# Kernel tuning notes

Measured on AMD Instinct MI355X. Metric: run time of the kernel, lower is better.

## Reference

```python
import jax, jax.numpy as jnp
import numpy as np

B, N, C, H = 2, 2048, 1024, 16
D = C // H  # head_dim = 64
ROPE_THETA = 500000.0
INIT_STD = 0.02


def setup_inputs() -> dict:
    key = jax.random.key(0)
    ks = jax.random.split(key, 6)
    hidden_states = jax.random.normal(ks[0], (B, N, C), dtype=jnp.float32)
    # rotary embeddings: standard llama-style, built from rope_theta
    inv_freq = jnp.asarray(1.0 / (ROPE_THETA ** (np.arange(0, D, 2, dtype=np.float32) / D)), jnp.float32)
    freqs = jnp.outer(jnp.arange(N, dtype=jnp.float32), inv_freq)  # (N, D/2)
    emb = jnp.concatenate([freqs, freqs], axis=-1)  # (N, D)
    cos = jnp.broadcast_to(jnp.cos(emb)[None], (B, N, D))
    sin = jnp.broadcast_to(jnp.sin(emb)[None], (B, N, D))
    Wq = jax.random.normal(ks[1], (C, C), jnp.float32) * INIT_STD
    Wk = jax.random.normal(ks[2], (C, C), jnp.float32) * INIT_STD
    Wv = jax.random.normal(ks[3], (C, C), jnp.float32) * INIT_STD
    Wo = jax.random.normal(ks[4], (C, C), jnp.float32) * INIT_STD
    return {"hidden_states": hidden_states, "cos": cos, "sin": sin,
            "Wq": Wq, "Wk": Wk, "Wv": Wv, "Wo": Wo}


def _rotate_half(x):
    x1, x2 = x[..., : D // 2], x[..., D // 2 :]
    return jnp.concatenate((-x2, x1), axis=-1)


def reference(hidden_states, cos, sin, Wq, Wk, Wv, Wo):
    scaling = D ** -0.5
    # projections; W stored as (in, out) so y = x @ W
    q = (hidden_states @ Wq) * scaling
    k = hidden_states @ Wk
    v = hidden_states @ Wv
    q = q.reshape(B, N, H, D)
    k = k.reshape(B, N, H, D)
    v = v.reshape(B, N, H, D)
    # RoPE, cos/sin broadcast over heads: (B,N,1,D)
    c = cos[:, :, None, :]
    s = sin[:, :, None, :]
    q = q * c + _rotate_half(q) * s
    k = k * c + _rotate_half(k) * s
    # causal SDPA (q already scaled)
    scores = jnp.einsum("bqhd,bkhd->bhqk", q, k)  # (B,H,N,N)
    causal = jnp.tril(jnp.ones((N, N), dtype=bool))
    scores = jnp.where(causal[None, None], scores, jnp.finfo(scores.dtype).min)
    probs = jax.nn.softmax(scores, axis=-1)
    out = jnp.einsum("bhqk,bkhd->bqhd", probs, v).reshape(B, N, C)
    return out @ Wo
```

## Files before the change

kernel.cpp:

```cpp
#include <hip/hip_runtime.h>
#include <hip/hip_bf16.h>

typedef __hip_bfloat16 bf16;
typedef __attribute__((ext_vector_type(8))) short short8;
typedef __attribute__((ext_vector_type(4))) short short4v;
typedef __attribute__((ext_vector_type(4))) float f32x4;

#define BB 2
#define NN 2048
#define CC 1024
#define HH 16
#define DD 64
#define MM (BB*NN)
#define QKVN 3072
#define LOG2E 1.44269504088896340736f

__device__ __forceinline__ void glds16(const void* g, void* l) {
    __builtin_amdgcn_global_load_lds((const __attribute__((address_space(1))) void*)g,
                                     (__attribute__((address_space(3))) void*)l, 16, 0, 0);
}
__device__ __forceinline__ short pkbf(float x) { bf16 t = (bf16)x; return *(short*)&t; }
__device__ __forceinline__ float b2f(short s) {
    return __uint_as_float(((unsigned)(unsigned short)s) << 16);
}

__global__ __launch_bounds__(256) void prep_fused(const float* __restrict__ hs,
                                                  const float* __restrict__ W0,
                                                  const float* __restrict__ W1,
                                                  const float* __restrict__ W2,
                                                  const float* __restrict__ W3,
                                                  bf16* __restrict__ hsb,
                                                  bf16* __restrict__ Wtqkv,
                                                  bf16* __restrict__ Wto) {
    __shared__ float t[32][33];
    const int bid = blockIdx.x;
    if (bid < 4096) {
        const int i = bid * 256 + threadIdx.x;
        float4 v = ((const float4*)hs)[i];
        short4v s;
        s.x = pkbf(v.x); s.y = pkbf(v.y); s.z = pkbf(v.z); s.w = pkbf(v.w);
        *((short4v*)hsb + i) = s;
    } else {
        const int b2 = bid - 4096;
        const int z = b2 >> 10;
        const float* W = z == 0 ? W0 : (z == 1 ? W1 : (z == 2 ? W2 : W3));
        bf16* dst = z < 3 ? Wtqkv + (size_t)z * CC * CC : Wto;
        const int bx = b2 & 31, by = (b2 >> 5) & 31;
        const int tx = threadIdx.x & 31, ty = threadIdx.x >> 5;
        const int x0 = bx * 32, y0 = by * 32;
        #pragma unroll
        for (int i = 0; i < 4; ++i)
            t[ty + i * 8][tx] = W[(size_t)(y0 + ty + i * 8) * CC + x0 + tx];
        __syncthreads();
        #pragma unroll
        for (int i = 0; i < 4; ++i)
            dst[(size_t)(x0 + ty + i * 8) * CC + y0 + tx] = (bf16)t[tx][ty + i * 8];
    }
}

__global__ __launch_bounds__(256) void gemm4qkv(const bf16* __restrict__ A,
                                                const bf16* __restrict__ Bt,
                                                bf16* __restrict__ Cb,
                                                const float* __restrict__ cosp,
                                                const float* __restrict__ sinp,
                                                bf16* __restrict__ VtOut) {
    __shared__ __align__(16) bf16 As[3][128 * 32];
    __shared__ __align__(16) bf16 Bs[3][128 * 32];
    const int tid = threadIdx.x, lane = tid & 63, wid = tid >> 6;
    const int wr = wid >> 1, wc = wid & 1, l16 = lane & 15, lg = lane >> 4;
    const int n0 = blockIdx.x * 128, m0 = blockIdx.y * 128;

    f32x4 acc[4][4];
    #pragma unroll
    for (int i = 0; i < 4; ++i)
        #pragma unroll
        for (int j = 0; j < 4; ++j) acc[i][j] = {0.f, 0.f, 0.f, 0.f};

    const int issue0 = wid * 2;
    const int sr0 = (issue0 * 1024 + lane * 16) >> 6;
    const int sc0 = ((issue0 * 1024 + lane * 16) & 63) >> 1;
    const int sr1 = ((issue0 + 1) * 1024 + lane * 16) >> 6;
    const int sc1 = (((issue0 + 1) * 1024 + lane * 16) & 63) >> 1;

    auto stage = [&](int k0, int bufi) {
        glds16(&A [(size_t)(m0 + sr0) * 1024 + k0 + sc0], (char*)&As[bufi][0] + issue0 * 1024);
        glds16(&Bt[(size_t)(n0 + sr0) * 1024 + k0 + sc0], (char*)&Bs[bufi][0] + issue0 * 1024);
        glds16(&A [(size_t)(m0 + sr1) * 1024 + k0 + sc1], (char*)&As[bufi][0] + (issue0 + 1) * 1024);
        glds16(&Bt[(size_t)(n0 + sr1) * 1024 + k0 + sc1], (char*)&Bs[bufi][0] + (issue0 + 1) * 1024);
    };

    stage(0, 0);
    stage(32, 1);
    int cur = 0, sb = 2;
    for (int t = 0; t < 32; ++t) {
        asm volatile("s_waitcnt vmcnt(4)" ::: "memory");
        __builtin_amdgcn_s_barrier();
        __builtin_amdgcn_sched_barrier(0);
        if (t + 2 < 32) stage((t + 2) * 32, sb);
        short8 af[4], bfr[4];
        #pragma unroll
        for (int i = 0; i < 4; ++i) af[i]  = *(const short8*)((char*)&As[cur][0] + (wr * 64 + i * 16 + l16) * 64 + lg * 16);
        #pragma unroll
        for (int j = 0; j < 4; ++j) bfr[j] = *(const short8*)((char*)&Bs[cur][0] + (wc * 64 + j * 16 + l16) * 64 + lg * 16);
        #pragma unroll
        for (int i = 0; i < 4; ++i)
            #pragma unroll
            for (int j = 0; j < 4; ++j)
                acc[i][j] = __builtin_amdgcn_mfma_f32_16x16x32_bf16(af[i], bfr[j], acc[i][j], 0, 0, 0);
        cur = (cur == 2) ? 0 : cur + 1;
        sb  = (sb  == 2) ? 0 : sb  + 1;
    }

    if (n0 >= 2 * CC) {
        #pragma unroll
        for (int i = 0; i < 4; ++i) {
            const int row0 = m0 + wr * 64 + i * 16 + lg * 4;
            const int bb = row0 >> 11, nn_ = row0 & (NN - 1);
            #pragma unroll
            for (int j = 0; j < 4; ++j) {
                const int col = n0 - 2 * CC + wc * 64 + j * 16 + l16;
                const int hh = col >> 6, d = col & 63;
                short4v s4;
                #pragma unroll
                for (int r = 0; r < 4; ++r) s4[r] = pkbf(acc[i][j][r]);
                *(short4v*)&VtOut[((size_t)(bb * HH + hh) * DD + d) * NN + nn_] = s4;
            }
        }
    } else {
        const float qs = (n0 < CC) ? 0.125f * LOG2E : 1.0f;
        #pragma unroll
        for (int i = 0; i < 4; ++i)
            #pragma unroll
            for (int r = 0; r < 4; ++r) {
                const int row = m0 + wr * 64 + i * 16 + lg * 4 + r;
                #pragma unroll
                for (int j = 0; j < 2; ++j) {
                    const int d = j * 16 + l16;
                    const float cv = cosp[(size_t)row * DD + d];
                    const float sv = sinp[(size_t)row * DD + d];
                    const float x1 = acc[i][j][r];
                    const float x2 = acc[i][j + 2][r];
                    const size_t cbase = (size_t)row * QKVN + n0 + wc * 64 + j * 16 + l16;
                    Cb[cbase]      = (bf16)((x1 * cv - x2 * sv) * qs);
                    Cb[cbase + 32] = (bf16)((x2 * cv + x1 * sv) * qs);
                }
            }
    }
}

__global__ __launch_bounds__(256) void gemm4o(const bf16* __restrict__ A,
                                              const bf16* __restrict__ Bt,
                                              float* __restrict__ Cf) {
    __shared__ __align__(16) bf16 As[3][64 * 32];
    __shared__ __align__(16) bf16 Bs[3][128 * 32];
    const int tid = threadIdx.x, lane = tid & 63, wid = tid >> 6;
    const int wr = wid >> 1, wc = wid & 1, l16 = lane & 15, lg = lane >> 4;
    const int n0 = blockIdx.x * 128, m0 = blockIdx.y * 64;

    f32x4 acc[2][4];
    #pragma unroll
    for (int i = 0; i < 2; ++i)
        #pragma unroll
        for (int j = 0; j < 4; ++j) acc[i][j] = {0.f, 0.f, 0.f, 0.f};

    const int asr = tid >> 2, asc = (tid & 3) * 8;
    const int issue0 = wid * 2;
    const int sr0 = (issue0 * 1024 + lane * 16) >> 6;
    const int sc0 = ((issue0 * 1024 + lane * 16) & 63) >> 1;
    const int sr1 = ((issue0 + 1) * 1024 + lane * 16) >> 6;
    const int sc1 = (((issue0 + 1) * 1024 + lane * 16) & 63) >> 1;

    auto stage = [&](int k0, int bufi) {
        glds16(&A [(size_t)(m0 + asr) * 1024 + k0 + asc], (char*)&As[bufi][0] + tid * 16);
        glds16(&Bt[(size_t)(n0 + sr0) * 1024 + k0 + sc0], (char*)&Bs[bufi][0] + issue0 * 1024);
        glds16(&Bt[(size_t)(n0 + sr1) * 1024 + k0 + sc1], (char*)&Bs[bufi][0] + (issue0 + 1) * 1024);
    };

    stage(0, 0);
    stage(32, 1);
    int cur = 0, sb = 2;
    for (int t = 0; t < 32; ++t) {
        asm volatile("s_waitcnt vmcnt(3)" ::: "memory");
        __builtin_amdgcn_s_barrier();
        __builtin_amdgcn_sched_barrier(0);
        if (t + 2 < 32) stage((t + 2) * 32, sb);
        short8 af[2], bfr[4];
        #pragma unroll
        for (int i = 0; i < 2; ++i) af[i]  = *(const short8*)((char*)&As[cur][0] + (wr * 32 + i * 16 + l16) * 64 + lg * 16);
        #pragma unroll
        for (int j = 0; j < 4; ++j) bfr[j] = *(const short8*)((char*)&Bs[cur][0] + (wc * 64 + j * 16 + l16) * 64 + lg * 16);
        #pragma unroll
        for (int i = 0; i < 2; ++i)
            #pragma unroll
            for (int j = 0; j < 4; ++j)
                acc[i][j] = __builtin_amdgcn_mfma_f32_16x16x32_bf16(af[i], bfr[j], acc[i][j], 0, 0, 0);
        cur = (cur == 2) ? 0 : cur + 1;
        sb  = (sb  == 2) ? 0 : sb  + 1;
    }

    #pragma unroll
    for (int i = 0; i < 2; ++i)
        #pragma unroll
        for (int r = 0; r < 4; ++r) {
            const int row = m0 + wr * 32 + i * 16 + lg * 4 + r;
            #pragma unroll
            for (int j = 0; j < 4; ++j)
                Cf[(size_t)row * CC + n0 + wc * 64 + j * 16 + l16] = acc[i][j][r];
        }
}

__global__ __launch_bounds__(256) void flash_mfma6(const bf16* __restrict__ QKV,
                                                   const bf16* __restrict__ Vt,
                                                   bf16* __restrict__ PartA,
                                                   bf16* __restrict__ PartB,
                                                   bf16* __restrict__ PartC,
                                                   float2* __restrict__ Mlb) {
    __shared__ __align__(16) bf16 Ks[2][4096];
    __shared__ __align__(16) bf16 Vs[2][4096];
    const int tid = threadIdx.x, lane = tid & 63, wid = tid >> 6;
    const int l16 = lane & 15, lg = lane >> 4;
    const int bid = blockIdx.x;
    const int bh = bid & 31;
    const int slot = bid >> 5;
    const int qt = 31 - slot / 3;
    const int part = slot % 3;
    const int h = bh & (HH - 1), b = bh >> 4;
    const int wq0 = qt * 64 + wid * 16;
    const int nkt = qt + 1;
    const int t0 = (part * nkt) / 3;
    const int cnt = ((part + 1) * nkt) / 3 - t0;
    const int grow = b * NN + wq0 + l16;

    const bf16* Kbase = QKV + (size_t)b * NN * QKVN + CC + h * DD;
    const bf16* Vbase = Vt + (size_t)(b * HH + h) * DD * NN;

    short8 qf[2];
    #pragma unroll
    for (int ch = 0; ch < 2; ++ch)
        qf[ch] = *(const short8*)&QKV[(size_t)grow * QKVN + h * DD + ch * 32 + lg * 8];

    f32x4 o[4];
    #pragma unroll
    for (int dn = 0; dn < 4; ++dn) o[dn] = {0.f, 0.f, 0.f, 0.f};
    float mx = -1e30f, ls = 0.f;

    const int a0 = (wid * 2) * 1024 + lane * 16, a1 = a0 + 1024;
    const int r0 = a0 >> 7, c0 = ((a0 & 127) ^ ((r0 & 7) << 4)) >> 1;
    const int r1 = a1 >> 7, c1 = ((a1 & 127) ^ ((r1 & 7) << 4)) >> 1;
    const bf16* kp0 = Kbase + (size_t)(t0 * 64 + r0) * QKVN + c0;
    const bf16* kp1 = Kbase + (size_t)(t0 * 64 + r1) * QKVN + c1;
    const bf16* vp0 = Vbase + (size_t)r0 * NN + t0 * 64 + c0;
    const bf16* vp1 = Vbase + (size_t)r1 * NN + t0 * 64 + c1;
    char* ldsK = (char*)&Ks[0][0] + wid * 2048;
    char* ldsV = (char*)&Vs[0][0] + wid * 2048;

    auto stage = [&](int par) {
        glds16(kp0, ldsK + par * 8192);
        glds16(kp1, ldsK + par * 8192 + 1024);
        glds16(vp0, ldsV + par * 8192);
        glds16(vp1, ldsV + par * 8192 + 1024);
        kp0 += 64 * QKVN; kp1 += 64 * QKVN; vp0 += 64; vp1 += 64;
    };

    if (cnt > 0) stage(0);
    for (int i = 0; i < cnt; ++i) {
        __syncthreads();
        if (i + 1 < cnt) stage((i + 1) & 1);
        const int cur = i & 1;
        const int kt = t0 + i;
        const int k0 = kt * 64;

        f32x4 st[4];
        #pragma unroll
        for (int kc = 0; kc < 4; ++kc) st[kc] = {0.f, 0.f, 0.f, 0.f};
        __builtin_amdgcn_s_setprio(1);
        #pragma unroll
        for (int kc = 0; kc < 4; ++kc) {
            const int row = kc * 16 + l16;
            const char* rb = (const char*)&Ks[cur][0] + row * 128;
            const int sw = (row & 7) << 4;
            short8 kf0 = *(const short8*)(rb + ((lg * 16) ^ sw));
            short8 kf1 = *(const short8*)(rb + ((64 + lg * 16) ^ sw));
            st[kc] = __builtin_amdgcn_mfma_f32_16x16x32_bf16(kf0, qf[0], st[kc], 0, 0, 0);
            st[kc] = __builtin_amdgcn_mfma_f32_16x16x32_bf16(kf1, qf[1], st[kc], 0, 0, 0);
        }
        __builtin_amdgcn_s_setprio(0);

        if (kt == qt) {
            #pragma unroll
            for (int kc = 0; kc < 4; ++kc)
                #pragma unroll
                for (int r = 0; r < 4; ++r)
                    if (k0 + kc * 16 + lg * 4 + r > wq0 + l16) st[kc][r] = -1e30f;
        }

        float rm = fmaxf(fmaxf(st[0][0], st[0][1]), fmaxf(st[0][2], st[0][3]));
        #pragma unroll
        for (int kc = 1; kc < 4; ++kc)
            rm = fmaxf(rm, fmaxf(fmaxf(st[kc][0], st[kc][1]), fmaxf(st[kc][2], st[kc][3])));
        if (__any(rm > mx + 8.0f)) {
            float wmx = fmaxf(rm, __shfl_xor(rm, 16, 64));
            wmx = fmaxf(wmx, __shfl_xor(wmx, 32, 64));
            const float mn = fmaxf(mx, wmx);
            const float sc = __builtin_amdgcn_exp2f(mx - mn);
            ls *= sc;
            #pragma unroll
            for (int dn = 0; dn < 4; ++dn) {
                o[dn][0] *= sc; o[dn][1] *= sc; o[dn][2] *= sc; o[dn][3] *= sc;
            }
            mx = mn;
        }
        float rs = 0.f;
        #pragma unroll
        for (int kc = 0; kc < 4; ++kc)
            #pragma unroll
            for (int r = 0; r < 4; ++r) {
                const float p = __builtin_amdgcn_exp2f(st[kc][r] - mx);
                st[kc][r] = p; rs += p;
            }
        ls += rs;

        __builtin_amdgcn_s_setprio(1);
        #pragma unroll
        for (int kc = 0; kc < 4; ++kc) {
            short4v pf;
            pf[0] = pkbf(st[kc][0]); pf[1] = pkbf(st[kc][1]);
            pf[2] = pkbf(st[kc][2]); pf[3] = pkbf(st[kc][3]);
            #pragma unroll
            for (int dn = 0; dn < 4; ++dn) {
                const int row = dn * 16 + l16;
                short4v vf = *(const short4v*)((const char*)&Vs[cur][0] + row * 128
                                               + ((kc * 32 + lg * 8) ^ ((row & 7) << 4)));
                o[dn] = __builtin_amdgcn_mfma_f32_16x16x16bf16_1k(vf, pf, o[dn], 0, 0, 0);
            }
        }
        __builtin_amdgcn_s_setprio(0);
    }

    ls += __shfl_xor(ls, 16, 64);
    ls += __shfl_xor(ls, 32, 64);
    if (lg == 0) Mlb[((size_t)(part * MM) + grow) * HH + h] = make_float2(mx, ls);
    bf16* dst = part == 0 ? PartA : (part == 1 ? PartB : PartC);
    const size_t rowb = (size_t)grow * CC + h * DD;
    #pragma unroll
    for (int dn = 0; dn < 4; ++dn) {
        short4v s4;
        s4[0] = pkbf(o[dn][0]); s4[1] = pkbf(o[dn][1]);
        s4[2] = pkbf(o[dn][2]); s4[3] = pkbf(o[dn][3]);
        *(short4v*)&dst[rowb + dn * 16 + lg * 4] = s4;
    }
}

__global__ __launch_bounds__(256) void merge3(const bf16* __restrict__ pa,
                                              const bf16* __restrict__ pb,
                                              const bf16* __restrict__ pc,
                                              const float2* __restrict__ ml,
                                              bf16* __restrict__ outp) {
    const int idx = blockIdx.x * 256 + threadIdx.x;
    const int row = idx >> 7;
    const int h = (idx & 127) >> 3;
    const float2 a  = ml[(size_t)row * HH + h];
    const float2 b_ = ml[((size_t)MM + row) * HH + h];
    const float2 c  = ml[((size_t)2 * MM + row) * HH + h];
    const float M = fmaxf(fmaxf(a.x, b_.x), c.x);
    const float w0 = (a.y  > 0.f) ? __builtin_amdgcn_exp2f(a.x  - M) : 0.f;
    const float w1 = (b_.y > 0.f) ? __builtin_amdgcn_exp2f(b_.x - M) : 0.f;
    const float w2 = (c.y  > 0.f) ? __builtin_amdgcn_exp2f(c.x  - M) : 0.f;
    const float inv = 1.f / (a.y * w0 + b_.y * w1 + c.y * w2);
    const float f0 = w0 * inv, f1 = w1 * inv, f2 = w2 * inv;
    const size_t off = (size_t)idx * 8;
    short8 va = *(const short8*)(pa + off);
    short8 vb = *(const short8*)(pb + off);
    short8 vc = *(const short8*)(pc + off);
    short8 ov;
    #pragma unroll
    for (int e = 0; e < 8; ++e)
        ov[e] = pkbf(b2f(va[e]) * f0 + b2f(vb[e]) * f1 + b2f(vc[e]) * f2);
    *(short8*)(outp + off) = ov;
}

extern "C" void kernel_launch(void* const* d_in, const int* in_sizes, int n_in,
                              void* d_out, int out_size, void* d_ws, size_t ws_size,
                              hipStream_t stream) {
    const float* hs   = (const float*)d_in[0];
    const float* cosp = (const float*)d_in[1];
    const float* sinp = (const float*)d_in[2];
    const float* Wq   = (const float*)d_in[3];
    const float* Wk   = (const float*)d_in[4];
    const float* Wv   = (const float*)d_in[5];
    const float* Wo   = (const float*)d_in[6];
    float* out = (float*)d_out;

    char* ws = (char*)d_ws;
    bf16* hsb   = (bf16*)(ws);
    bf16* Wtqkv = (bf16*)(ws + (8  << 20));
    bf16* Wto   = (bf16*)(ws + (14 << 20));
    bf16* QKV   = (bf16*)(ws + (16 << 20));
    bf16* Vtb   = (bf16*)(ws + (40 << 20));
    bf16* Abuf  = hsb;
    float2* Mlb = (float2*)Wtqkv;
    bf16* PartB = (bf16*)out;
    bf16* PartC = (bf16*)out + (size_t)MM * CC;

    prep_fused<<<8192, 256, 0, stream>>>(hs, Wq, Wk, Wv, Wo, hsb, Wtqkv, Wto);

    gemm4qkv<<<dim3(QKVN / 128, MM / 128), 256, 0, stream>>>(
        hsb, Wtqkv, QKV, cosp, sinp, Vtb);

    flash_mfma6<<<3072, 256, 0, stream>>>(QKV, Vtb, Abuf, PartB, PartC, Mlb);

    merge3<<<2048, 256, 0, stream>>>(Abuf, PartB, PartC, Mlb, Abuf);

    gemm4o<<<dim3(CC / 128, MM / 64), 256, 0, stream>>>(Abuf, Wto, out);
}
```

Measured before the change: 116.3 us.

## Use 32-key tiles in flash attention and skip fully masked tiles per wave

The flash attention kernel now iterates over 32-key tiles instead of 64-key tiles, halving shared memory per buffer and using one async global-to-LDS load per thread per tile for K and V. Each wave skips compute for tiles lying entirely above its own 16 causal query rows, and masking only applies on diagonal-crossing tiles. This cuts wasted MFMA and exp work on the causal diagonal, but doubles loop iterations and __syncthreads barriers per unit of work and gives less compute per barrier.

```diff
diff --git a/kernel.cpp b/kernel.cpp
--- a/kernel.cpp
+++ b/kernel.cpp
@@ -209,14 +209,14 @@
         }
 }
 
-__global__ __launch_bounds__(256) void flash_mfma6(const bf16* __restrict__ QKV,
-                                                   const bf16* __restrict__ Vt,
-                                                   bf16* __restrict__ PartA,
-                                                   bf16* __restrict__ PartB,
-                                                   bf16* __restrict__ PartC,
-                                                   float2* __restrict__ Mlb) {
-    __shared__ __align__(16) bf16 Ks[2][4096];
-    __shared__ __align__(16) bf16 Vs[2][4096];
+__global__ __launch_bounds__(256) void flash_mfma10(const bf16* __restrict__ QKV,
+                                                    const bf16* __restrict__ Vt,
+                                                    bf16* __restrict__ PartA,
+                                                    bf16* __restrict__ PartB,
+                                                    bf16* __restrict__ PartC,
+                                                    float2* __restrict__ Mlb) {
+    __shared__ __align__(16) bf16 Ks[2][2048];
+    __shared__ __align__(16) bf16 Vs[2][2048];
     const int tid = threadIdx.x, lane = tid & 63, wid = tid >> 6;
     const int l16 = lane & 15, lg = lane >> 4;
     const int bid = blockIdx.x;
@@ -226,7 +226,7 @@
     const int part = slot % 3;
     const int h = bh & (HH - 1), b = bh >> 4;
     const int wq0 = qt * 64 + wid * 16;
-    const int nkt = qt + 1;
+    const int nkt = 2 * qt + 2;
     const int t0 = (part * nkt) / 3;
     const int cnt = ((part + 1) * nkt) / 3 - t0;
     const int grow = b * NN + wq0 + l16;
@@ -244,22 +244,17 @@
     for (int dn = 0; dn < 4; ++dn) o[dn] = {0.f, 0.f, 0.f, 0.f};
     float mx = -1e30f, ls = 0.f;
 
-    const int a0 = (wid * 2) * 1024 + lane * 16, a1 = a0 + 1024;
-    const int r0 = a0 >> 7, c0 = ((a0 & 127) ^ ((r0 & 7) << 4)) >> 1;
-    const int r1 = a1 >> 7, c1 = ((a1 & 127) ^ ((r1 & 7) << 4)) >> 1;
-    const bf16* kp0 = Kbase + (size_t)(t0 * 64 + r0) * QKVN + c0;
-    const bf16* kp1 = Kbase + (size_t)(t0 * 64 + r1) * QKVN + c1;
-    const bf16* vp0 = Vbase + (size_t)r0 * NN + t0 * 64 + c0;
-    const bf16* vp1 = Vbase + (size_t)r1 * NN + t0 * 64 + c1;
-    char* ldsK = (char*)&Ks[0][0] + wid * 2048;
-    char* ldsV = (char*)&Vs[0][0] + wid * 2048;
+    const int kr = tid >> 3;
+    const int kcb = ((tid & 7) * 16) ^ ((kr & 7) << 4);
+    const int vr = tid >> 2;
+    const int vcb = ((tid & 3) * 16) ^ ((vr & 3) << 4);
+    const bf16* kp = Kbase + (size_t)(t0 * 32 + kr) * QKVN + (kcb >> 1);
+    const bf16* vp = Vbase + (size_t)vr * NN + t0 * 32 + (vcb >> 1);
 
     auto stage = [&](int par) {
-        glds16(kp0, ldsK + par * 8192);
-        glds16(kp1, ldsK + par * 8192 + 1024);
-        glds16(vp0, ldsV + par * 8192);
-        glds16(vp1, ldsV + par * 8192 + 1024);
-        kp0 += 64 * QKVN; kp1 += 64 * QKVN; vp0 += 64; vp1 += 64;
+        glds16(kp, (char*)&Ks[par][0] + tid * 16);
+        glds16(vp, (char*)&Vs[par][0] + tid * 16);
+        kp += 32 * QKVN; vp += 32;
     };
 
     if (cnt > 0) stage(0);
@@ -267,74 +262,73 @@
         __syncthreads();
         if (i + 1 < cnt) stage((i + 1) & 1);
         const int cur = i & 1;
-        const int kt = t0 + i;
-        const int k0 = kt * 64;
-
-        f32x4 st[4];
-        #pragma unroll
-        for (int kc = 0; kc < 4; ++kc) st[kc] = {0.f, 0.f, 0.f, 0.f};
-        __builtin_amdgcn_s_setprio(1);
-        #pragma unroll
-        for (int kc = 0; kc < 4; ++kc) {
-            const int row = kc * 16 + l16;
-            const char* rb = (const char*)&Ks[cur][0] + row * 128;
-            const int sw = (row & 7) << 4;
-            short8 kf0 = *(const short8*)(rb + ((lg * 16) ^ sw));
-            short8 kf1 = *(const short8*)(rb + ((64 + lg * 16) ^ sw));
-            st[kc] = __builtin_amdgcn_mfma_f32_16x16x32_bf16(kf0, qf[0], st[kc], 0, 0, 0);
-            st[kc] = __builtin_amdgcn_mfma_f32_16x16x32_bf16(kf1, qf[1], st[kc], 0, 0, 0);
+        const int k0 = (t0 + i) * 32;
+
+        if (k0 <= wq0 + 15) {
+            f32x4 st[2];
+            #pragma unroll
+            for (int kc = 0; kc < 2; ++kc) st[kc] = {0.f, 0.f, 0.f, 0.f};
+            __builtin_amdgcn_s_setprio(1);
+            #pragma unroll
+            for (int kc = 0; kc < 2; ++kc) {
+                const int row = kc * 16 + l16;
+                const char* rb = (const char*)&Ks[cur][0] + row * 128;
+                const int sw = (row & 7) << 4;
+                short8 kf0 = *(const short8*)(rb + ((lg * 16) ^ sw));
+                short8 kf1 = *(const short8*)(rb + ((64 + lg * 16) ^ sw));
+                st[kc] = __builtin_amdgcn_mfma_f32_16x16x32_bf16(kf0, qf[0], st[kc], 0, 0, 0);
+                st[kc] = __builtin_amdgcn_mfma_f32_16x16x32_bf16(kf1, qf[1], st[kc], 0, 0, 0);
+            }
+            __builtin_amdgcn_s_setprio(0);
+
+            if (k0 + 31 > wq0) {
+                #pragma unroll
+                for (int kc = 0; kc < 2; ++kc)
+                    #pragma unroll
+                    for (int r = 0; r < 4; ++r)
+                        if (k0 + kc * 16 + lg * 4 + r > wq0 + l16) st[kc][r] = -1e30f;
+            }
+
+            float rm = fmaxf(fmaxf(st[0][0], st[0][1]), fmaxf(st[0][2], st[0][3]));
+            rm = fmaxf(rm, fmaxf(fmaxf(st[1][0], st[1][1]), fmaxf(st[1][2], st[1][3])));
+            if (__any(rm > mx + 8.0f)) {
+                float wmx = fmaxf(rm, __shfl_xor(rm, 16, 64));
+                wmx = fmaxf(wmx, __shfl_xor(wmx, 32, 64));
+                const float mn = fmaxf(mx, wmx);
+                const float sc = __builtin_amdgcn_exp2f(mx - mn);
+                ls *= sc;
+                #pragma unroll
+                for (int dn = 0; dn < 4; ++dn) {
+                    o[dn][0] *= sc; o[dn][1] *= sc; o[dn][2] *= sc; o[dn][3] *= sc;
+                }
+                mx = mn;
+            }
+            float rs = 0.f;
+            #pragma unroll
+            for (int kc = 0; kc < 2; ++kc)
+                #pragma unroll
+                for (int r = 0; r < 4; ++r) {
+                    const float p = __builtin_amdgcn_exp2f(st[kc][r] - mx);
+                    st[kc][r] = p; rs += p;
+                }
+            ls += rs;
+
+            __builtin_amdgcn_s_setprio(1);
+            #pragma unroll
+            for (int kc = 0; kc < 2; ++kc) {
+                short4v pf;
+                pf[0] = pkbf(st[kc][0]); pf[1] = pkbf(st[kc][1]);
+                pf[2] = pkbf(st[kc][2]); pf[3] = pkbf(st[kc][3]);
+                #pragma unroll
+                for (int dn = 0; dn < 4; ++dn) {
+                    const int row = dn * 16 + l16;
+                    short4v vf = *(const short4v*)((const char*)&Vs[cur][0] + row * 64
+                                                   + ((kc * 32 + lg * 8) ^ ((row & 3) << 4)));
+                    o[dn] = __builtin_amdgcn_mfma_f32_16x16x16bf16_1k(vf, pf, o[dn], 0, 0, 0);
+                }
+            }
+            __builtin_amdgcn_s_setprio(0);
         }
-        __builtin_amdgcn_s_setprio(0);
-
-        if (kt == qt) {
-            #pragma unroll
-            for (int kc = 0; kc < 4; ++kc)
-                #pragma unroll
-                for (int r = 0; r < 4; ++r)
-                    if (k0 + kc * 16 + lg * 4 + r > wq0 + l16) st[kc][r] = -1e30f;
-        }
-
-        float rm = fmaxf(fmaxf(st[0][0], st[0][1]), fmaxf(st[0][2], st[0][3]));
-        #pragma unroll
-        for (int kc = 1; kc < 4; ++kc)
-            rm = fmaxf(rm, fmaxf(fmaxf(st[kc][0], st[kc][1]), fmaxf(st[kc][2], st[kc][3])));
-        if (__any(rm > mx + 8.0f)) {
-            float wmx = fmaxf(rm, __shfl_xor(rm, 16, 64));
-            wmx = fmaxf(wmx, __shfl_xor(wmx, 32, 64));
-            const float mn = fmaxf(mx, wmx);
-            const float sc = __builtin_amdgcn_exp2f(mx - mn);
-            ls *= sc;
-            #pragma unroll
-            for (int dn = 0; dn < 4; ++dn) {
-                o[dn][0] *= sc; o[dn][1] *= sc; o[dn][2] *= sc; o[dn][3] *= sc;
-            }
-            mx = mn;
-        }
-        float rs = 0.f;
-        #pragma unroll
-        for (int kc = 0; kc < 4; ++kc)
-            #pragma unroll
-            for (int r = 0; r < 4; ++r) {
-                const float p = __builtin_amdgcn_exp2f(st[kc][r] - mx);
-                st[kc][r] = p; rs += p;
-            }
-        ls += rs;
-
-        __builtin_amdgcn_s_setprio(1);
-        #pragma unroll
-        for (int kc = 0; kc < 4; ++kc) {
-            short4v pf;
-            pf[0] = pkbf(st[kc][0]); pf[1] = pkbf(st[kc][1]);
-            pf[2] = pkbf(st[kc][2]); pf[3] = pkbf(st[kc][3]);
-            #pragma unroll
-            for (int dn = 0; dn < 4; ++dn) {
-                const int row = dn * 16 + l16;
-                short4v vf = *(const short4v*)((const char*)&Vs[cur][0] + row * 128
-                                               + ((kc * 32 + lg * 8) ^ ((row & 7) << 4)));
-                o[dn] = __builtin_amdgcn_mfma_f32_16x16x16bf16_1k(vf, pf, o[dn], 0, 0, 0);
-            }
-        }
-        __builtin_amdgcn_s_setprio(0);
     }
 
     ls += __shfl_xor(ls, 16, 64);
@@ -407,7 +401,7 @@
     gemm4qkv<<<dim3(QKVN / 128, MM / 128), 256, 0, stream>>>(
         hsb, Wtqkv, QKV, cosp, sinp, Vtb);
 
-    flash_mfma6<<<3072, 256, 0, stream>>>(QKV, Vtb, Abuf, PartB, PartC, Mlb);
+    flash_mfma10<<<3072, 256, 0, stream>>>(QKV, Vtb, Abuf, PartB, PartC, Mlb);
 
     merge3<<<2048, 256, 0, stream>>>(Abuf, PartB, PartC, Mlb, Abuf);
 
```

After: 124.1 us. +6.8%, slower.
